# Kernel tuning notes

Hardware: AMD Instinct MI355X
Metric: run time of the kernel (lower is better)

Reference implementation:

```python
import jax, jax.numpy as jnp
import numpy as np

B, N, H, HEADS, F, L = 32, 256, 512, 8, 2048, 8
D = H // HEADS  # per-head dim
EPS = 1e-5


def _layernorm(x, scale, bias):
    mu = jnp.mean(x, axis=-1, keepdims=True)
    var = jnp.mean(jnp.square(x - mu), axis=-1, keepdims=True)
    return (x - mu) * jax.lax.rsqrt(var + EPS) * scale + bias


def setup_inputs() -> dict:
    key = jax.random.key(0)
    ks = jax.random.split(key, 12)
    s = 0.02
    inp = {
        "x": jax.random.normal(ks[0], (B, N, H), jnp.float32),
        "attn_bias": jax.random.normal(ks[1], (B, HEADS, N, N), jnp.float32),
        "ln1_s": jnp.ones((L, H), jnp.float32),
        "ln1_b": jnp.zeros((L, H), jnp.float32),
        "wq": s * jax.random.normal(ks[2], (L, H, H), jnp.float32),
        "bq": jnp.zeros((L, H), jnp.float32),
        "wk": s * jax.random.normal(ks[3], (L, H, H), jnp.float32),
        "bk": jnp.zeros((L, H), jnp.float32),
        "wv": s * jax.random.normal(ks[4], (L, H, H), jnp.float32),
        "bv": jnp.zeros((L, H), jnp.float32),
        "wo": s * jax.random.normal(ks[5], (L, H, H), jnp.float32),
        "bo": jnp.zeros((L, H), jnp.float32),
        "ln2_s": jnp.ones((L, H), jnp.float32),
        "ln2_b": jnp.zeros((L, H), jnp.float32),
        "w1": s * jax.random.normal(ks[6], (L, H, F), jnp.float32),
        "b1": jnp.zeros((L, F), jnp.float32),
        "w2": s * jax.random.normal(ks[7], (L, F, H), jnp.float32),
        "b2": jnp.zeros((L, H), jnp.float32),
    }
    return inp


def reference(x, attn_bias, ln1_s, ln1_b, wq, bq, wk, bk, wv, bv, wo, bo,
              ln2_s, ln2_b, w1, b1, w2, b2):
    scale = D ** (-0.5)
    for l in range(L):
        # --- self attention block ---
        y = _layernorm(x, ln1_s[l], ln1_b[l])
        q = (y @ wq[l] + bq[l]).reshape(B, N, HEADS, D) * scale
        k = (y @ wk[l] + bk[l]).reshape(B, N, HEADS, D)
        v = (y @ wv[l] + bv[l]).reshape(B, N, HEADS, D)
        scores = jnp.einsum("bqhd,bkhd->bhqk", q, k) + attn_bias
        probs = jax.nn.softmax(scores, axis=-1)
        ctx = jnp.einsum("bhqk,bkhd->bqhd", probs, v).reshape(B, N, H)
        x = x + ctx @ wo[l] + bo[l]
        # --- FFN block ---
        y = _layernorm(x, ln2_s[l], ln2_b[l])
        y = jax.nn.gelu(y @ w1[l] + b1[l], approximate=False)
        x = x + y @ w2[l] + b2[l]
    return x
```

## Files before the change

kernel.cpp:

```cpp
#include <hip/hip_runtime.h>
#include <hip/hip_bf16.h>
#include <math.h>

typedef __bf16 bf16;
typedef __bf16 bf16x8 __attribute__((ext_vector_type(8)));
typedef __bf16 bf16x4 __attribute__((ext_vector_type(4)));
typedef float  f32x4  __attribute__((ext_vector_type(4)));

#define DEV __device__ __forceinline__

DEV f32x4 mfma16(bf16x8 a, bf16x8 b, f32x4 c) {
    return __builtin_amdgcn_mfma_f32_16x16x32_bf16(a, b, c, 0, 0, 0);
}

DEV void gload16(const bf16* g, bf16* l) {
    __builtin_amdgcn_global_load_lds(
        (const __attribute__((address_space(1))) void*)g,
        (__attribute__((address_space(3))) void*)l, 16, 0, 0);
}

DEV float gelu_f(float v) {
    float xs = v * 0.70710678118654752f;
    float ax = fabsf(xs);
    float t  = 1.0f / (1.0f + 0.3275911f * ax);
    float p  = t * (0.254829592f + t * (-0.284496736f + t * (1.421413741f +
               t * (-1.453152027f + t * 1.061405429f))));
    float er = 1.0f - p * __expf(-ax * ax);
    er = copysignf(er, xs);
    return 0.5f * v * (1.0f + er);
}

template <int MODE>
__global__ __launch_bounds__(256, 3) void gemm_k(
    const bf16* __restrict__ A, const bf16* __restrict__ Bt,
    const float* __restrict__ bias, bf16* __restrict__ Cb,
    bf16* __restrict__ vt, int K, int ldC)
{
    __shared__ bf16 smem[(MODE == 2) ? 17408 : 16384];
    bf16* As = smem;
    bf16* Bs = smem + 8192;

    const int tid  = threadIdx.x;
    const int lane = tid & 63;
    const int w    = tid >> 6;
    const int wm   = w & 1, wn = w >> 1;
    const long tm  = (long)blockIdx.y * 128;
    const long tn  = (long)blockIdx.x * 128;

    f32x4 acc[4][4] = {};

    const int r0 = tid >> 2;
    const int cc = ((tid & 3) ^ ((r0 >> 1) & 3)) * 8;
    const bf16* Ag = A  + (tm + r0) * K + cc;
    const bf16* Bg = Bt + (tn + r0) * K + cc;
    const long rstep = (long)64 * K;

    int am[4], bn[4];
#pragma unroll
    for (int i = 0; i < 4; ++i) {
        int ra = wm * 64 + i * 16 + (lane & 15);
        am[i]  = ra * 32 + (((lane >> 4) ^ ((ra >> 1) & 3)) * 8);
        int rb = wn * 64 + i * 16 + (lane & 15);
        bn[i]  = rb * 32 + (((lane >> 4) ^ ((rb >> 1) & 3)) * 8);
    }

#define STAGE(buf, kk)                                        \
    do {                                                      \
        gload16(Ag + (kk),         &As[(buf)*4096 + tid*8]);  \
        gload16(Ag + rstep + (kk), &As[(buf)*4096 + 2048 + tid*8]); \
        gload16(Bg + (kk),         &Bs[(buf)*4096 + tid*8]);  \
        gload16(Bg + rstep + (kk), &Bs[(buf)*4096 + 2048 + tid*8]); \
    } while (0)

#define COMPUTE(buf)                                                    \
    do {                                                                \
        bf16x8 a[4], b[4];                                              \
        _Pragma("unroll")                                               \
        for (int i = 0; i < 4; ++i) a[i] = *(const bf16x8*)&As[(buf)*4096 + am[i]]; \
        _Pragma("unroll")                                               \
        for (int i = 0; i < 4; ++i) b[i] = *(const bf16x8*)&Bs[(buf)*4096 + bn[i]]; \
        _Pragma("unroll")                                               \
        for (int mi = 0; mi < 4; ++mi)                                  \
            _Pragma("unroll")                                           \
            for (int ni = 0; ni < 4; ++ni)                              \
                acc[mi][ni] = mfma16(a[mi], b[ni], acc[mi][ni]);        \
    } while (0)

    STAGE(0, 0);
    __syncthreads();
    for (int k0 = 0; k0 < K; k0 += 64) {
        STAGE(1, k0 + 32);
        COMPUTE(0);
        __syncthreads();
        if (k0 + 64 < K) STAGE(0, k0 + 64);
        COMPUTE(1);
        __syncthreads();
    }

    bool vpath = false;
    if constexpr (MODE == 2) vpath = (tn >= 1024);

    if (vpath) {
        bf16* Ct = smem;
#pragma unroll
        for (int mi = 0; mi < 4; ++mi) {
            const int rowL = wm * 64 + mi * 16 + ((lane >> 4) << 2);
#pragma unroll
            for (int ni = 0; ni < 4; ++ni) {
                const int colL = wn * 64 + ni * 16 + (lane & 15);
                const float bv = bias[tn + colL];
                bf16x4 pk;
#pragma unroll
                for (int r = 0; r < 4; ++r) pk[r] = (bf16)(acc[mi][ni][r] + bv);
                *(bf16x4*)&Ct[colL * 136 + rowL] = pk;
            }
        }
        __syncthreads();
        const int b_blk = (int)(tm >> 8);
        const int nin   = (int)(tm & 255);
        const int cvb   = (int)(tn - 1024);
#pragma unroll
        for (int j = 0; j < 8; ++j) {
            int idx = j * 256 + tid;
            int c   = idx >> 4;
            int nc  = (idx & 15) * 8;
            bf16x8 vv = *(const bf16x8*)&Ct[c * 136 + nc];
            int cv = cvb + c;
            *(bf16x8*)&vt[(((long)b_blk * 8 + (cv >> 6)) * 64 + (cv & 63)) * 256 + nin + nc] = vv;
        }
        return;
    }

#pragma unroll
    for (int mi = 0; mi < 4; ++mi) {
        const long rbase = tm + wm * 64 + mi * 16 + ((lane >> 4) << 2);
#pragma unroll
        for (int ni = 0; ni < 4; ++ni) {
            const long col = tn + wn * 64 + ni * 16 + (lane & 15);
            const float bv = bias[col];
#pragma unroll
            for (int r = 0; r < 4; ++r) {
                float v = acc[mi][ni][r] + bv;
                if constexpr (MODE == 1) v = gelu_f(v);
                Cb[(rbase + r) * (long)ldC + col] = (bf16)v;
            }
        }
    }
#undef STAGE
#undef COMPUTE
}

__global__ __launch_bounds__(256, 3) void gemm_dk(
    const bf16* __restrict__ A, const bf16* __restrict__ Bt,
    bf16* __restrict__ D, int K, int Ks)
{
    __shared__ bf16 smem[16384];
    bf16* As = smem;
    bf16* Bs = smem + 8192;

    const int tid  = threadIdx.x;
    const int lane = tid & 63;
    const int w    = tid >> 6;
    const int wm   = w & 1, wn = w >> 1;
    const long tm  = (long)blockIdx.y * 128;
    const long tn  = (long)blockIdx.x * 128;
    const int kbase = blockIdx.z * Ks;

    f32x4 acc[4][4] = {};

    const int r0 = tid >> 2;
    const int cc = ((tid & 3) ^ ((r0 >> 1) & 3)) * 8;
    const bf16* Ag = A  + (tm + r0) * K + kbase + cc;
    const bf16* Bg = Bt + (tn + r0) * K + kbase + cc;
    const long rstep = (long)64 * K;

    int am[4], bn[4];
#pragma unroll
    for (int i = 0; i < 4; ++i) {
        int ra = wm * 64 + i * 16 + (lane & 15);
        am[i]  = ra * 32 + (((lane >> 4) ^ ((ra >> 1) & 3)) * 8);
        int rb = wn * 64 + i * 16 + (lane & 15);
        bn[i]  = rb * 32 + (((lane >> 4) ^ ((rb >> 1) & 3)) * 8);
    }

#define STAGE(buf, kk)                                        \
    do {                                                      \
        gload16(Ag + (kk),         &As[(buf)*4096 + tid*8]);  \
        gload16(Ag + rstep + (kk), &As[(buf)*4096 + 2048 + tid*8]); \
        gload16(Bg + (kk),         &Bs[(buf)*4096 + tid*8]);  \
        gload16(Bg + rstep + (kk), &Bs[(buf)*4096 + 2048 + tid*8]); \
    } while (0)

#define COMPUTE(buf)                                                    \
    do {                                                                \
        bf16x8 a[4], b[4];                                              \
        _Pragma("unroll")                                               \
        for (int i = 0; i < 4; ++i) a[i] = *(const bf16x8*)&As[(buf)*4096 + am[i]]; \
        _Pragma("unroll")                                               \
        for (int i = 0; i < 4; ++i) b[i] = *(const bf16x8*)&Bs[(buf)*4096 + bn[i]]; \
        _Pragma("unroll")                                               \
        for (int mi = 0; mi < 4; ++mi)                                  \
            _Pragma("unroll")                                           \
            for (int ni = 0; ni < 4; ++ni)                              \
                acc[mi][ni] = mfma16(a[mi], b[ni], acc[mi][ni]);        \
    } while (0)

    STAGE(0, 0);
    __syncthreads();
    for (int k0 = 0; k0 < Ks; k0 += 64) {
        STAGE(1, k0 + 32);
        COMPUTE(0);
        __syncthreads();
        if (k0 + 64 < Ks) STAGE(0, k0 + 64);
        COMPUTE(1);
        __syncthreads();
    }

    bf16* Dp = D + (long)blockIdx.z * 8192 * 512;
#pragma unroll
    for (int mi = 0; mi < 4; ++mi) {
        const long rbase = tm + wm * 64 + mi * 16 + ((lane >> 4) << 2);
#pragma unroll
        for (int ni = 0; ni < 4; ++ni) {
            const long col = tn + wn * 64 + ni * 16 + (lane & 15);
#pragma unroll
            for (int r = 0; r < 4; ++r)
                Dp[(rbase + r) * 512 + col] = (bf16)acc[mi][ni][r];
        }
    }
#undef STAGE
#undef COMPUTE
}

__global__ __launch_bounds__(256, 4) void attn_k(
    const bf16* __restrict__ qkv, const bf16* __restrict__ vt,
    const float* __restrict__ bias, bf16* __restrict__ ctx)
{
    __shared__ bf16 smem[256 * 72];
    bf16* Ks = smem;

    const int tid = threadIdx.x, lane = tid & 63, w = tid >> 6;
    const int qt = blockIdx.x & 3;
    const int h  = (blockIdx.x >> 2) & 7;
    const int b  = blockIdx.x >> 5;
    const long qkv_base = (long)b * 256 * 1536;

#pragma unroll
    for (int i = 0; i < 8; ++i) {
        int p = i * 256 + tid;
        int n = p >> 3, kk = (p & 7) * 8;
        uint4 v = *(const uint4*)(qkv + qkv_base + (long)n * 1536 + 512 + h * 64 + kk);
        *(uint4*)&Ks[n * 72 + kk] = v;
    }

    const int qr0 = qt * 64 + w * 16;
    bf16x8 aq0, aq1;
    {
        const bf16* g = qkv + qkv_base + (long)(qr0 + (lane & 15)) * 1536 + h * 64 + ((lane >> 4) * 8);
        aq0 = *(const bf16x8*)g;
        aq1 = *(const bf16x8*)(g + 32);
    }
    __syncthreads();

    f32x4 s[16];
    const float* bb = bias + (((long)(b * 8 + h)) * 256 + qr0) * 256;
#pragma unroll
    for (int ct = 0; ct < 16; ++ct) {
        const int col = ct * 16 + (lane & 15);
        f32x4 c;
#pragma unroll
        for (int r = 0; r < 4; ++r)
            c[r] = bb[(long)((lane >> 4) * 4 + r) * 256 + col];
        bf16x8 k0 = *(const bf16x8*)&Ks[(ct * 16 + (lane & 15)) * 72 + ((lane >> 4) * 8)];
        bf16x8 k1 = *(const bf16x8*)&Ks[(ct * 16 + (lane & 15)) * 72 + 32 + ((lane >> 4) * 8)];
        c = mfma16(aq0, k0, c);
        c = mfma16(aq1, k1, c);
        s[ct] = c;
    }

    float m[4] = {-1e30f, -1e30f, -1e30f, -1e30f};
#pragma unroll
    for (int ct = 0; ct < 16; ++ct)
#pragma unroll
        for (int r = 0; r < 4; ++r) m[r] = fmaxf(m[r], s[ct][r]);
#pragma unroll
    for (int r = 0; r < 4; ++r)
#pragma unroll
        for (int off = 1; off < 16; off <<= 1)
            m[r] = fmaxf(m[r], __shfl_xor(m[r], off));
    float l[4] = {0.f, 0.f, 0.f, 0.f};
#pragma unroll
    for (int ct = 0; ct < 16; ++ct)
#pragma unroll
        for (int r = 0; r < 4; ++r) {
            float p = __expf(s[ct][r] - m[r]);
            s[ct][r] = p;
            l[r] += p;
        }
#pragma unroll
    for (int r = 0; r < 4; ++r) {
#pragma unroll
        for (int off = 1; off < 16; off <<= 1) l[r] += __shfl_xor(l[r], off);
        l[r] = 1.0f / l[r];
    }

    __syncthreads();
    bf16* P = smem + w * (16 * 264);
#pragma unroll
    for (int ct = 0; ct < 16; ++ct)
#pragma unroll
        for (int r = 0; r < 4; ++r)
            P[(long)((lane >> 4) * 4 + r) * 264 + ct * 16 + (lane & 15)] = (bf16)s[ct][r];

    bf16x8 ap[8];
#pragma unroll
    for (int nk = 0; nk < 8; ++nk)
        ap[nk] = *(const bf16x8*)&P[(lane & 15) * 264 + nk * 32 + (lane >> 4) * 8];

    const bf16* vg = vt + (long)(b * 8 + h) * 64 * 256;
    f32x4 o[4];
#pragma unroll
    for (int dt = 0; dt < 4; ++dt) {
        f32x4 c = {};
#pragma unroll
        for (int nk = 0; nk < 8; ++nk) {
            bf16x8 bv = *(const bf16x8*)&vg[(dt * 16 + (lane & 15)) * 256 + nk * 32 + (lane >> 4) * 8];
            c = mfma16(ap[nk], bv, c);
        }
        o[dt] = c;
    }

#pragma unroll
    for (int dt = 0; dt < 4; ++dt) {
        const int col = h * 64 + dt * 16 + (lane & 15);
#pragma unroll
        for (int r = 0; r < 4; ++r) {
            const long row = (long)b * 256 + qr0 + (lane >> 4) * 4 + r;
            ctx[row * 512 + col] = (bf16)(o[dt][r] * l[r]);
        }
    }
}

template <int NS>
__global__ __launch_bounds__(256) void ln_k(
    const float* __restrict__ x, float* __restrict__ xout,
    const bf16* __restrict__ d, const float* __restrict__ rbias,
    const float* __restrict__ sc, const float* __restrict__ bi,
    bf16* __restrict__ y)
{
    const int lane = threadIdx.x & 63;
    const long row = (long)blockIdx.x * 4 + (threadIdx.x >> 6);
    const float* xr = x + row * 512;
    float v[8];
    *(float4*)&v[0] = ((const float4*)xr)[lane * 2];
    *(float4*)&v[4] = ((const float4*)xr)[lane * 2 + 1];
    if constexpr (NS == 2) {
        bf16x8 d0 = *(const bf16x8*)&d[row * 512 + lane * 8];
        bf16x8 d1 = *(const bf16x8*)&d[(long)8192 * 512 + row * 512 + lane * 8];
        float b4[8];
        *(float4*)&b4[0] = ((const float4*)rbias)[lane * 2];
        *(float4*)&b4[4] = ((const float4*)rbias)[lane * 2 + 1];
#pragma unroll
        for (int j = 0; j < 8; ++j)
            v[j] += (float)d0[j] + (float)d1[j] + b4[j];
        float* xo = xout + row * 512;
        ((float4*)xo)[lane * 2]     = *(const float4*)&v[0];
        ((float4*)xo)[lane * 2 + 1] = *(const float4*)&v[4];
    }
    float sum = 0.f;
#pragma unroll
    for (int j = 0; j < 8; ++j) sum += v[j];
#pragma unroll
    for (int off = 1; off < 64; off <<= 1) sum += __shfl_xor(sum, off);
    const float mu = sum * (1.0f / 512.0f);
    float sq = 0.f;
#pragma unroll
    for (int j = 0; j < 8; ++j) { float dd = v[j] - mu; sq += dd * dd; }
#pragma unroll
    for (int off = 1; off < 64; off <<= 1) sq += __shfl_xor(sq, off);
    const float rs = rsqrtf(sq * (1.0f / 512.0f) + 1e-5f);
    bf16* yr = y + row * 512;
#pragma unroll
    for (int j = 0; j < 8; ++j) {
        int c = lane * 8 + j;
        yr[c] = (bf16)((v[j] - mu) * rs * sc[c] + bi[c]);
    }
}

__global__ __launch_bounds__(256) void addout_k(
    const float* __restrict__ x, const bf16* __restrict__ d,
    const float* __restrict__ rbias, float* __restrict__ out)
{
    const int lane = threadIdx.x & 63;
    const long row = (long)blockIdx.x * 4 + (threadIdx.x >> 6);
    float v[8];
    *(float4*)&v[0] = ((const float4*)(x + row * 512))[lane * 2];
    *(float4*)&v[4] = ((const float4*)(x + row * 512))[lane * 2 + 1];
    bf16x8 d0 = *(const bf16x8*)&d[row * 512 + lane * 8];
    bf16x8 d1 = *(const bf16x8*)&d[(long)8192 * 512 + row * 512 + lane * 8];
    float b4[8];
    *(float4*)&b4[0] = ((const float4*)rbias)[lane * 2];
    *(float4*)&b4[4] = ((const float4*)rbias)[lane * 2 + 1];
#pragma unroll
    for (int j = 0; j < 8; ++j)
        v[j] += (float)d0[j] + (float)d1[j] + b4[j];
    float* o = out + row * 512;
    ((float4*)o)[lane * 2]     = *(const float4*)&v[0];
    ((float4*)o)[lane * 2 + 1] = *(const float4*)&v[4];
}

__global__ __launch_bounds__(256) void transpose_k(
    const float* __restrict__ wq, const float* __restrict__ wk,
    const float* __restrict__ wv, const float* __restrict__ wo,
    const float* __restrict__ w1, const float* __restrict__ w2,
    bf16* __restrict__ qkvT, bf16* __restrict__ woT,
    bf16* __restrict__ w1T, bf16* __restrict__ w2T)
{
    __shared__ float tile[32][33];
    const int tid = threadIdx.x, tx = tid & 31, ty = tid >> 5;
    const int l = blockIdx.x / 3072;
    const int r = blockIdx.x % 3072;

    const float* In = nullptr;
    bf16* Out = nullptr;
    int Nd, tk, tn, rowOff = 0, ldO;
    float scale = 1.0f;
    if (r < 1024) {
        const int which = r >> 8, t = r & 255;
        tn = t >> 4; tk = t & 15; Nd = 512; ldO = 512;
        const long woff = (long)l * 512 * 512;
        if (which == 0)      { In = wq + woff; Out = qkvT + (long)l * 1536 * 512; rowOff = 0;    scale = 0.125f; }
        else if (which == 1) { In = wk + woff; Out = qkvT + (long)l * 1536 * 512; rowOff = 512;  }
        else if (which == 2) { In = wv + woff; Out = qkvT + (long)l * 1536 * 512; rowOff = 1024; }
        else                 { In = wo + woff; Out = woT + woff; }
    } else if (r < 2048) {
        const int t = r - 1024;
        tn = t >> 4; tk = t & 15; Nd = 2048; ldO = 512;
        In = w1 + (long)l * 512 * 2048; Out = w1T + (long)l * 2048 * 512;
    } else {
        const int t = r - 2048;
        tn = t & 15; tk = t >> 4; Nd = 512; ldO = 2048;
        In = w2 + (long)l * 2048 * 512; Out = w2T + (long)l * 512 * 2048;
    }
    const int gk = tk * 32, gn = tn * 32;
#pragma unroll
    for (int j = 0; j < 4; ++j) {
        int rr = ty + j * 8;
        tile[rr][tx] = In[(long)(gk + rr) * Nd + gn + tx] * scale;
    }
    __syncthreads();
#pragma unroll
    for (int j = 0; j < 4; ++j) {
        int rr = ty + j * 8;
        Out[(long)(rowOff + gn + rr) * ldO + gk + tx] = (bf16)tile[tx][rr];
    }
}

__global__ void biasq_k(const float* __restrict__ bq, const float* __restrict__ bk,
                        const float* __restrict__ bv, float* __restrict__ bqkv)
{
    int i = blockIdx.x * 256 + threadIdx.x;
    if (i >= 8 * 1536) return;
    int l = i / 1536, j = i % 1536;
    float v;
    if (j < 512)       v = bq[l * 512 + j] * 0.125f;
    else if (j < 1024) v = bk[l * 512 + j - 512];
    else               v = bv[l * 512 + j - 1024];
    bqkv[i] = v;
}

extern "C" void kernel_launch(void* const* d_in, const int* in_sizes, int n_in,
                              void* d_out, int out_size, void* d_ws, size_t ws_size,
                              hipStream_t stream)
{
    (void)in_sizes; (void)n_in; (void)out_size; (void)ws_size;
    const float* x    = (const float*)d_in[0];
    const float* ab   = (const float*)d_in[1];
    const float* ln1s = (const float*)d_in[2];
    const float* ln1b = (const float*)d_in[3];
    const float* wq   = (const float*)d_in[4];
    const float* bq   = (const float*)d_in[5];
    const float* wk   = (const float*)d_in[6];
    const float* bk   = (const float*)d_in[7];
    const float* wv   = (const float*)d_in[8];
    const float* bv   = (const float*)d_in[9];
    const float* wo   = (const float*)d_in[10];
    const float* bo   = (const float*)d_in[11];
    const float* ln2s = (const float*)d_in[12];
    const float* ln2b = (const float*)d_in[13];
    const float* w1   = (const float*)d_in[14];
    const float* b1   = (const float*)d_in[15];
    const float* w2   = (const float*)d_in[16];
    const float* b2   = (const float*)d_in[17];

    char* ws = (char*)d_ws;
    float* xf   = (float*)ws;
    bf16* y     = (bf16*)(ws + 16777216);
    bf16* ctx   = y;
    bf16* qkv   = (bf16*)(ws + 16777216 + 8388608);
    bf16* ffn   = qkv;
    bf16* vt    = qkv + (long)8192 * 1536;
    bf16* dbuf  = (bf16*)(ws + 16777216 + 8388608 + 33554432);
    bf16* wqkvT = dbuf + (long)2 * 8192 * 512;
    bf16* woT   = wqkvT + (long)8 * 1536 * 512;
    bf16* w1T   = woT + (long)8 * 512 * 512;
    bf16* w2T   = w1T + (long)8 * 2048 * 512;
    float* bqkv = (float*)(w2T + (long)8 * 512 * 2048);

    hipMemcpyAsync(xf, x, (size_t)8192 * 512 * 4, hipMemcpyDeviceToDevice, stream);
    transpose_k<<<24576, 256, 0, stream>>>(wq, wk, wv, wo, w1, w2, wqkvT, woT, w1T, w2T);
    biasq_k<<<48, 256, 0, stream>>>(bq, bk, bv, bqkv);

    for (int l = 0; l < 8; ++l) {
        if (l == 0)
            ln_k<0><<<2048, 256, 0, stream>>>(xf, nullptr, nullptr, nullptr,
                                              ln1s, ln1b, y);
        else
            ln_k<2><<<2048, 256, 0, stream>>>(xf, xf, dbuf, b2 + (l - 1) * 512,
                                              ln1s + l * 512, ln1b + l * 512, y);
        gemm_k<2><<<dim3(12, 64), 256, 0, stream>>>(
            y, wqkvT + (long)l * 1536 * 512, bqkv + l * 1536, qkv, vt, 512, 1536);
        attn_k<<<1024, 256, 0, stream>>>(qkv, vt, ab, ctx);
        gemm_dk<<<dim3(4, 64, 2), 256, 0, stream>>>(
            ctx, woT + (long)l * 512 * 512, dbuf, 512, 256);
        ln_k<2><<<2048, 256, 0, stream>>>(xf, xf, dbuf, bo + l * 512,
                                          ln2s + l * 512, ln2b + l * 512, y);
        gemm_k<1><<<dim3(16, 64), 256, 0, stream>>>(
            y, w1T + (long)l * 2048 * 512, b1 + l * 2048, ffn, nullptr, 512, 2048);
        gemm_dk<<<dim3(4, 64, 2), 256, 0, stream>>>(
            ffn, w2T + (long)l * 512 * 2048, dbuf, 2048, 1024);
    }
    addout_k<<<2048, 256, 0, stream>>>(xf, dbuf, b2 + 7 * 512, (float*)d_out);
}
```

Measured before the change: 1.358 ms.

## Narrow split-K GEMM tiles and transpose attention scores for vectorized bias loads

The split-K output GEMM now uses 128x64 tiles instead of 128x128. That doubles the grid, shrinks shared memory and accumulators, and raises the launch-bounds occupancy hint, at the cost of less B-operand reuse per tile. The attention kernel swaps the MFMA operands so each lane holds one query row's scores. This lets the bias be loaded as float4 vectors, cuts the softmax reductions to two shuffles, and writes P as packed bf16x4 with normalization applied before the PV matmul. Normalizing before the bf16 cast changes rounding slightly.

```diff
diff --git a/kernel.cpp b/kernel.cpp
--- a/kernel.cpp
+++ b/kernel.cpp
@@ -150,11 +150,11 @@
 #undef COMPUTE
 }
 
-__global__ __launch_bounds__(256, 3) void gemm_dk(
+__global__ __launch_bounds__(256, 4) void gemm_dk(
     const bf16* __restrict__ A, const bf16* __restrict__ Bt,
     bf16* __restrict__ D, int K, int Ks)
 {
-    __shared__ bf16 smem[16384];
+    __shared__ bf16 smem[8192 + 4096];
     bf16* As = smem;
     bf16* Bs = smem + 8192;
 
@@ -163,10 +163,10 @@
     const int w    = tid >> 6;
     const int wm   = w & 1, wn = w >> 1;
     const long tm  = (long)blockIdx.y * 128;
-    const long tn  = (long)blockIdx.x * 128;
+    const long tn  = (long)blockIdx.x * 64;
     const int kbase = blockIdx.z * Ks;
 
-    f32x4 acc[4][4] = {};
+    f32x4 acc[4][2] = {};
 
     const int r0 = tid >> 2;
     const int cc = ((tid & 3) ^ ((r0 >> 1) & 3)) * 8;
@@ -174,12 +174,15 @@
     const bf16* Bg = Bt + (tn + r0) * K + kbase + cc;
     const long rstep = (long)64 * K;
 
-    int am[4], bn[4];
+    int am[4], bn[2];
 #pragma unroll
     for (int i = 0; i < 4; ++i) {
         int ra = wm * 64 + i * 16 + (lane & 15);
         am[i]  = ra * 32 + (((lane >> 4) ^ ((ra >> 1) & 3)) * 8);
-        int rb = wn * 64 + i * 16 + (lane & 15);
+    }
+#pragma unroll
+    for (int i = 0; i < 2; ++i) {
+        int rb = wn * 32 + i * 16 + (lane & 15);
         bn[i]  = rb * 32 + (((lane >> 4) ^ ((rb >> 1) & 3)) * 8);
     }
 
@@ -187,21 +190,20 @@
     do {                                                      \
         gload16(Ag + (kk),         &As[(buf)*4096 + tid*8]);  \
         gload16(Ag + rstep + (kk), &As[(buf)*4096 + 2048 + tid*8]); \
-        gload16(Bg + (kk),         &Bs[(buf)*4096 + tid*8]);  \
-        gload16(Bg + rstep + (kk), &Bs[(buf)*4096 + 2048 + tid*8]); \
+        gload16(Bg + (kk),         &Bs[(buf)*2048 + tid*8]);  \
     } while (0)
 
 #define COMPUTE(buf)                                                    \
     do {                                                                \
-        bf16x8 a[4], b[4];                                              \
+        bf16x8 a[4], b[2];                                              \
         _Pragma("unroll")                                               \
         for (int i = 0; i < 4; ++i) a[i] = *(const bf16x8*)&As[(buf)*4096 + am[i]]; \
         _Pragma("unroll")                                               \
-        for (int i = 0; i < 4; ++i) b[i] = *(const bf16x8*)&Bs[(buf)*4096 + bn[i]]; \
+        for (int i = 0; i < 2; ++i) b[i] = *(const bf16x8*)&Bs[(buf)*2048 + bn[i]]; \
         _Pragma("unroll")                                               \
         for (int mi = 0; mi < 4; ++mi)                                  \
             _Pragma("unroll")                                           \
-            for (int ni = 0; ni < 4; ++ni)                              \
+            for (int ni = 0; ni < 2; ++ni)                              \
                 acc[mi][ni] = mfma16(a[mi], b[ni], acc[mi][ni]);        \
     } while (0)
 
@@ -221,8 +223,8 @@
     for (int mi = 0; mi < 4; ++mi) {
         const long rbase = tm + wm * 64 + mi * 16 + ((lane >> 4) << 2);
 #pragma unroll
-        for (int ni = 0; ni < 4; ++ni) {
-            const long col = tn + wn * 64 + ni * 16 + (lane & 15);
+        for (int ni = 0; ni < 2; ++ni) {
+            const long col = tn + wn * 32 + ni * 16 + (lane & 15);
 #pragma unroll
             for (int r = 0; r < 4; ++r)
                 Dp[(rbase + r) * 512 + col] = (bf16)acc[mi][ni][r];
@@ -263,54 +265,48 @@
     __syncthreads();
 
     f32x4 s[16];
-    const float* bb = bias + (((long)(b * 8 + h)) * 256 + qr0) * 256;
+    const float* bq_ = bias + ((((long)(b * 8 + h)) * 256 + qr0 + (lane & 15)) * 256)
+                     + ((lane >> 4) * 4);
 #pragma unroll
     for (int ct = 0; ct < 16; ++ct) {
-        const int col = ct * 16 + (lane & 15);
-        f32x4 c;
-#pragma unroll
-        for (int r = 0; r < 4; ++r)
-            c[r] = bb[(long)((lane >> 4) * 4 + r) * 256 + col];
+        f32x4 c = *(const f32x4*)(bq_ + ct * 16);
         bf16x8 k0 = *(const bf16x8*)&Ks[(ct * 16 + (lane & 15)) * 72 + ((lane >> 4) * 8)];
         bf16x8 k1 = *(const bf16x8*)&Ks[(ct * 16 + (lane & 15)) * 72 + 32 + ((lane >> 4) * 8)];
-        c = mfma16(aq0, k0, c);
-        c = mfma16(aq1, k1, c);
+        c = mfma16(k0, aq0, c);
+        c = mfma16(k1, aq1, c);
         s[ct] = c;
     }
 
-    float m[4] = {-1e30f, -1e30f, -1e30f, -1e30f};
+    float m = -1e30f;
 #pragma unroll
     for (int ct = 0; ct < 16; ++ct)
 #pragma unroll
-        for (int r = 0; r < 4; ++r) m[r] = fmaxf(m[r], s[ct][r]);
-#pragma unroll
-    for (int r = 0; r < 4; ++r)
-#pragma unroll
-        for (int off = 1; off < 16; off <<= 1)
-            m[r] = fmaxf(m[r], __shfl_xor(m[r], off));
-    float l[4] = {0.f, 0.f, 0.f, 0.f};
+        for (int r = 0; r < 4; ++r) m = fmaxf(m, s[ct][r]);
+    m = fmaxf(m, __shfl_xor(m, 16));
+    m = fmaxf(m, __shfl_xor(m, 32));
+
+    float l = 0.f;
 #pragma unroll
     for (int ct = 0; ct < 16; ++ct)
 #pragma unroll
         for (int r = 0; r < 4; ++r) {
-            float p = __expf(s[ct][r] - m[r]);
+            float p = __expf(s[ct][r] - m);
             s[ct][r] = p;
-            l[r] += p;
-        }
-#pragma unroll
-    for (int r = 0; r < 4; ++r) {
-#pragma unroll
-        for (int off = 1; off < 16; off <<= 1) l[r] += __shfl_xor(l[r], off);
-        l[r] = 1.0f / l[r];
-    }
+            l += p;
+        }
+    l += __shfl_xor(l, 16);
+    l += __shfl_xor(l, 32);
+    const float linv = 1.0f / l;
 
     __syncthreads();
     bf16* P = smem + w * (16 * 264);
 #pragma unroll
-    for (int ct = 0; ct < 16; ++ct)
-#pragma unroll
-        for (int r = 0; r < 4; ++r)
-            P[(long)((lane >> 4) * 4 + r) * 264 + ct * 16 + (lane & 15)] = (bf16)s[ct][r];
+    for (int ct = 0; ct < 16; ++ct) {
+        bf16x4 pk;
+#pragma unroll
+        for (int r = 0; r < 4; ++r) pk[r] = (bf16)(s[ct][r] * linv);
+        *(bf16x4*)&P[(lane & 15) * 264 + ct * 16 + ((lane >> 4) * 4)] = pk;
+    }
 
     bf16x8 ap[8];
 #pragma unroll
@@ -336,7 +332,7 @@
 #pragma unroll
         for (int r = 0; r < 4; ++r) {
             const long row = (long)b * 256 + qr0 + (lane >> 4) * 4 + r;
-            ctx[row * 512 + col] = (bf16)(o[dt][r] * l[r]);
+            ctx[row * 512 + col] = (bf16)o[dt][r];
         }
     }
 }
@@ -521,13 +517,13 @@
         gemm_k<2><<<dim3(12, 64), 256, 0, stream>>>(
             y, wqkvT + (long)l * 1536 * 512, bqkv + l * 1536, qkv, vt, 512, 1536);
         attn_k<<<1024, 256, 0, stream>>>(qkv, vt, ab, ctx);
-        gemm_dk<<<dim3(4, 64, 2), 256, 0, stream>>>(
+        gemm_dk<<<dim3(8, 64, 2), 256, 0, stream>>>(
             ctx, woT + (long)l * 512 * 512, dbuf, 512, 256);
         ln_k<2><<<2048, 256, 0, stream>>>(xf, xf, dbuf, bo + l * 512,
                                           ln2s + l * 512, ln2b + l * 512, y);
         gemm_k<1><<<dim3(16, 64), 256, 0, stream>>>(
             y, w1T + (long)l * 2048 * 512, b1 + l * 2048, ffn, nullptr, 512, 2048);
-        gemm_dk<<<dim3(4, 64, 2), 256, 0, stream>>>(
+        gemm_dk<<<dim3(8, 64, 2), 256, 0, stream>>>(
             ffn, w2T + (long)l * 512 * 2048, dbuf, 2048, 1024);
     }
     addout_k<<<2048, 256, 0, stream>>>(xf, dbuf, b2 + 7 * 512, (float*)d_out);
```

After: 1.513 ms. 1.11x slower.
